# Kernel tuning notes

Hardware: AMD Instinct MI355X
Metric: run time of the kernel (lower is better)

The kernel has to match this reference:

```python
import jax, jax.numpy as jnp
import numpy as np

SPATIAL_SHAPES = [(100, 100), (50, 50), (25, 25), (13, 13)]  # (h, w) per level
D_MODEL, N_HEADS, N_LEVELS, N_POINTS = 256, 8, 4, 4
B = 2
S = sum(h * w for h, w in SPATIAL_SHAPES)  # 13294
Q = S  # encoder self-attention: num_queries == sequence_length


def setup_inputs() -> dict:
    key = jax.random.key(0)
    ks = jax.random.split(key, 12)
    d = D_MODEL
    hlp = N_HEADS * N_LEVELS * N_POINTS
    scale = 0.02
    starts = np.cumsum([0] + [h * w for h, w in SPATIAL_SHAPES[:-1]])
    return {
        "hidden_states": jax.random.normal(ks[0], (B, Q, d), jnp.float32),
        "encoder_hidden_states": jax.random.normal(ks[1], (B, S, d), jnp.float32),
        "reference_points": jax.random.uniform(ks[2], (B, Q, N_LEVELS, 2), jnp.float32),
        "W_value": jax.random.normal(ks[3], (d, d), jnp.float32) * scale,
        "b_value": jnp.zeros((d,), jnp.float32),
        "W_off": jax.random.normal(ks[4], (d, hlp * 2), jnp.float32) * scale,
        "b_off": jax.random.normal(ks[5], (hlp * 2,), jnp.float32) * scale,
        "W_attn": jax.random.normal(ks[6], (d, hlp), jnp.float32) * scale,
        "b_attn": jnp.zeros((hlp,), jnp.float32),
        "W_out": jax.random.normal(ks[7], (d, d), jnp.float32) * scale,
        "b_out": jnp.zeros((d,), jnp.float32),
        "spatial_shapes": jnp.asarray(SPATIAL_SHAPES, jnp.int32),
        "level_start_index": jnp.asarray(starts, jnp.int32),
    }


def bilinear_sample(img, grid):
    # img: [N, C, h, w]; grid: [N, Q, P, 2] xy in [-1, 1]
    # F.grid_sample(mode='bilinear', padding_mode='zeros', align_corners=False)
    N, C, h, w = img.shape
    Qg, Pg = grid.shape[1], grid.shape[2]
    x = ((grid[..., 0] + 1.0) * w - 1.0) * 0.5
    y = ((grid[..., 1] + 1.0) * h - 1.0) * 0.5
    x0 = jnp.floor(x)
    y0 = jnp.floor(y)
    x1 = x0 + 1.0
    y1 = y0 + 1.0
    wx1 = x - x0
    wx0 = 1.0 - wx1
    wy1 = y - y0
    wy0 = 1.0 - wy1
    img_flat = img.reshape(N, C, h * w)

    def gather(xi, yi):
        valid = (xi >= 0) & (xi <= w - 1) & (yi >= 0) & (yi <= h - 1)
        xi_c = jnp.clip(xi, 0, w - 1).astype(jnp.int32)
        yi_c = jnp.clip(yi, 0, h - 1).astype(jnp.int32)
        idx = (yi_c * w + xi_c).reshape(N, 1, Qg * Pg)
        vals = jnp.take_along_axis(img_flat, idx, axis=2)  # [N, C, Q*P]
        return vals * valid.reshape(N, 1, Qg * Pg).astype(img.dtype)

    out = (
        gather(x0, y0) * (wx0 * wy0).reshape(N, 1, -1)
        + gather(x1, y0) * (wx1 * wy0).reshape(N, 1, -1)
        + gather(x0, y1) * (wx0 * wy1).reshape(N, 1, -1)
        + gather(x1, y1) * (wx1 * wy1).reshape(N, 1, -1)
    )
    return out.reshape(N, C, Qg, Pg)


def reference(hidden_states, encoder_hidden_states, reference_points,
              W_value, b_value, W_off, b_off, W_attn, b_attn, W_out, b_out,
              spatial_shapes, level_start_index):
    Bq, Qn, d = hidden_states.shape
    H, L, P = N_HEADS, N_LEVELS, N_POINTS
    Dh = d // H
    value = (encoder_hidden_states @ W_value + b_value).reshape(Bq, -1, H, Dh)
    off = (hidden_states @ W_off + b_off).reshape(Bq, Qn, H, L, P, 2)
    aw = (hidden_states @ W_attn + b_attn).reshape(Bq, Qn, H, L * P)
    aw = jax.nn.softmax(aw, axis=-1).reshape(Bq, Qn, H, L, P)
    # offset normalizer is (width, height) per level
    norm = jnp.stack([spatial_shapes[:, 1], spatial_shapes[:, 0]], -1).astype(off.dtype)
    loc = reference_points[:, :, None, :, None, :] + off / norm[None, None, None, :, None, :]
    grids = 2.0 * loc - 1.0  # [B, Q, H, L, P, 2]

    starts = np.cumsum([0] + [h * w for h, w in SPATIAL_SHAPES])
    sampled = []
    for lvl, (h, w) in enumerate(SPATIAL_SHAPES):
        v = value[:, starts[lvl]:starts[lvl + 1]]              # [B, h*w, H, Dh]
        v = v.transpose(0, 2, 3, 1).reshape(Bq * H, Dh, h, w)   # [B*H, Dh, h, w]
        g = grids[:, :, :, lvl].transpose(0, 2, 1, 3, 4).reshape(Bq * H, Qn, P, 2)
        sampled.append(bilinear_sample(v, g))                   # [B*H, Dh, Q, P]
    samp = jnp.stack(sampled, axis=-2).reshape(Bq * H, Dh, Qn, L * P)
    wts = aw.transpose(0, 2, 1, 3, 4).reshape(Bq * H, 1, Qn, L * P)
    out = (samp * wts).sum(-1)                                  # [B*H, Dh, Q]
    out = out.reshape(Bq, H * Dh, Qn).transpose(0, 2, 1)        # [B, Q, d]
    out = out @ W_out + b_out
    return out, aw
```

## Files before the change

kernel.cpp:

```cpp
#include <hip/hip_runtime.h>
#include <hip/hip_bf16.h>
#include <math.h>

#define BQn 2
#define QN 13294
#define SN 13294
#define NH 8
#define DH 32
#define DM 256

typedef __attribute__((ext_vector_type(8))) short short8;
typedef __attribute__((ext_vector_type(4))) float f32x4;

__device__ __forceinline__ unsigned short f2bf(float x) {
    union { float f; unsigned int u; } c; c.f = x;
    unsigned int r = c.u + 0x7fff + ((c.u >> 16) & 1);
    return (unsigned short)(r >> 16);
}
__device__ __forceinline__ float asf(unsigned int u) {
    union { unsigned int i; float f; } c; c.i = u; return c.f;
}

__global__ __launch_bounds__(256) void conv_weights(
    const float* __restrict__ Wv, const float* __restrict__ Woff,
    const float* __restrict__ Wa, const float* __restrict__ Wout,
    unsigned short* __restrict__ WvT, unsigned short* __restrict__ WoffT,
    unsigned short* __restrict__ WaT, unsigned short* __restrict__ WoutT)
{
    const int t = blockIdx.x * 256 + threadIdx.x;
    if (t < 65536) {
        const int n = t & 255, k = t >> 8;
        WvT[(size_t)n * 256 + k] = f2bf(Wv[(size_t)k * 256 + n]);
    } else if (t < 131072) {
        const int i = t - 65536, n = i & 255, k = i >> 8;
        WoffT[(size_t)n * 256 + k] = f2bf(Woff[(size_t)k * 256 + n]);
    } else if (t < 163840) {
        const int i = t - 131072, n = i & 127, k = i >> 7;
        WaT[(size_t)n * 256 + k] = f2bf(Wa[(size_t)k * 128 + n]);
    } else if (t < 229376) {
        const int i = t - 163840, n = i & 255, k = i >> 8;
        WoutT[(size_t)n * 256 + k] = f2bf(Wout[(size_t)k * 256 + n]);
    }
}

template<int N, int MODE, bool AF32>
__global__ __launch_bounds__(256) void gemm_mfma(
    const void* __restrict__ Av,
    const unsigned short* __restrict__ WT,
    const float* __restrict__ bias0,
    const float* __restrict__ bias1,
    void* __restrict__ Cv, int M)
{
    __shared__ unsigned short As[128][72];
    __shared__ unsigned short Bs[64][72];
    const int tid  = threadIdx.x;
    const int lane = tid & 63, wid = tid >> 6;
    const int wr = wid >> 1, wc = wid & 1;
    const int r0 = blockIdx.y * 128, n0 = blockIdx.x * 64;

    f32x4 acc[4][2] = {};

    for (int k0 = 0; k0 < 256; k0 += 64) {
        #pragma unroll
        for (int i = 0; i < 4; ++i) {
            const int idx = i * 256 + tid;
            const int row = idx >> 3, ch = (idx & 7) << 3;
            int grow = r0 + row; if (grow >= M) grow = M - 1;
            if (AF32) {
                const float* Af = (const float*)Av;
                const float4 v0 = *(const float4*)(Af + (size_t)grow * 256 + k0 + ch);
                const float4 v1 = *(const float4*)(Af + (size_t)grow * 256 + k0 + ch + 4);
                union { __hip_bfloat162 b[4]; uint4 u; } pk;
                pk.b[0] = __float22bfloat162_rn(make_float2(v0.x, v0.y));
                pk.b[1] = __float22bfloat162_rn(make_float2(v0.z, v0.w));
                pk.b[2] = __float22bfloat162_rn(make_float2(v1.x, v1.y));
                pk.b[3] = __float22bfloat162_rn(make_float2(v1.z, v1.w));
                *(uint4*)&As[row][ch] = pk.u;
            } else {
                const unsigned short* Ab = (const unsigned short*)Av;
                *(uint4*)&As[row][ch] =
                    *(const uint4*)(Ab + (size_t)grow * 256 + k0 + ch);
            }
        }
        #pragma unroll
        for (int i = 0; i < 2; ++i) {
            const int idx = i * 256 + tid;
            const int row = idx >> 3, ch = (idx & 7) << 3;
            *(uint4*)&Bs[row][ch] =
                *(const uint4*)(WT + (size_t)(n0 + row) * 256 + k0 + ch);
        }
        __syncthreads();
        #pragma unroll
        for (int kk = 0; kk < 2; ++kk) {
            const int kb = kk * 32 + (lane >> 4) * 8;
            short8 bfr[2];
            #pragma unroll
            for (int n = 0; n < 2; ++n)
                bfr[n] = *(const short8*)&Bs[wc * 32 + n * 16 + (lane & 15)][kb];
            #pragma unroll
            for (int m = 0; m < 4; ++m) {
                const short8 afr =
                    *(const short8*)&As[wr * 64 + m * 16 + (lane & 15)][kb];
                #pragma unroll
                for (int n = 0; n < 2; ++n)
                    acc[m][n] = __builtin_amdgcn_mfma_f32_16x16x32_bf16(
                        afr, bfr[n], acc[m][n], 0, 0, 0);
            }
        }
        __syncthreads();
    }

    #pragma unroll
    for (int m = 0; m < 4; ++m)
        #pragma unroll
        for (int n = 0; n < 2; ++n) {
            const int col = n0 + wc * 32 + n * 16 + (lane & 15);
            const float bsv = (col < 256) ? bias0[col] : bias1[col - 256];
            #pragma unroll
            for (int j = 0; j < 4; ++j) {
                const int row = r0 + wr * 64 + m * 16 + (lane >> 4) * 4 + j;
                if (row >= M) continue;
                const float v = acc[m][n][j] + bsv;
                if (MODE == 0) {
                    ((float*)Cv)[(size_t)row * N + col] = v;
                } else {
                    const int b = (row >= SN), s = row - b * SN;
                    const int h = col >> 5, dh = col & 31;
                    ((unsigned short*)Cv)
                        [(((size_t)b * NH + h) * SN + s) * DH + dh] = f2bf(v);
                }
            }
        }
}

__global__ __launch_bounds__(256) void ms_sample(
    const unsigned short* __restrict__ value,
    const float* __restrict__ offaw,
    const float* __restrict__ refp,
    unsigned short* __restrict__ outh,
    float* __restrict__ awout)
{
    const int h  = blockIdx.x & 7;
    const int qc = blockIdx.x >> 3;
    const int lc = threadIdx.x & 7;
    const int bq = qc * 32 + (threadIdx.x >> 3);
    if (bq >= BQn * QN) return;
    const int b  = (bq >= QN);
    const int gbase = threadIdx.x & 56;

    const float* rowp = offaw + (size_t)bq * 384;

    const float2 lw2 = *(const float2*)(rowp + 256 + h * 16 + lc * 2);
    float m = fmaxf(lw2.x, lw2.y);
    #pragma unroll
    for (int d = 1; d < 8; d <<= 1) m = fmaxf(m, __shfl_xor(m, d, 8));
    float e0 = __expf(lw2.x - m), e1 = __expf(lw2.y - m);
    float s = e0 + e1;
    #pragma unroll
    for (int d = 1; d < 8; d <<= 1) s += __shfl_xor(s, d, 8);
    const float inv = 1.f / s;
    e0 *= inv; e1 *= inv;
    *(float2*)(awout + (size_t)bq * 128 + h * 16 + lc * 2) = make_float2(e0, e1);

    const float4 o4 = *(const float4*)(rowp + h * 32 + lc * 4);
    const int lvl = lc >> 1;
    const float2 rp = *(const float2*)(refp + (size_t)bq * 8 + lvl * 2);
    const float rw = (lvl == 0) ? 0.01f : (lvl == 1) ? 0.02f
                   : (lvl == 2) ? 0.04f : (1.0f / 13.0f);
    const float lx0 = fmaf(o4.x, rw, rp.x), ly0 = fmaf(o4.y, rw, rp.y);
    const float lx1 = fmaf(o4.z, rw, rp.x), ly1 = fmaf(o4.w, rw, rp.y);

    float ax = 0.f, ay = 0.f, az = 0.f, aw_ = 0.f;
    const unsigned short* vplane =
        value + (((size_t)b * NH + h) * SN) * DH + lc * 4;

    #pragma unroll
    for (int p = 0; p < 16; ++p) {
        constexpr int LW[4]  = {100, 50, 25, 13};
        constexpr int LST[4] = {0, 10000, 12500, 13125};
        const int l  = p >> 2;
        const int w  = LW[l];
        const int st = LST[l];
        const int src = gbase + (p >> 1);
        const float lx = __shfl((p & 1) ? lx1 : lx0, src, 64);
        const float ly = __shfl((p & 1) ? ly1 : ly0, src, 64);
        const float wt = __shfl((p & 1) ? e1  : e0,  src, 64);

        const float x = fmaf(lx, (float)w, -0.5f);
        const float y = fmaf(ly, (float)w, -0.5f);
        const float x0f = floorf(x), y0f = floorf(y);
        const int x0 = (int)x0f, y0 = (int)y0f;
        const float wx1 = x - x0f, wx0 = 1.f - wx1;
        const float wy1 = y - y0f, wy0 = 1.f - wy1;

        #pragma unroll
        for (int c = 0; c < 4; ++c) {
            const int xi = x0 + (c & 1);
            const int yi = y0 + (c >> 1);
            const float cw = ((c & 1) ? wx1 : wx0) * ((c >> 1) ? wy1 : wy0);
            const bool valid = ((unsigned)xi < (unsigned)w) &
                               ((unsigned)yi < (unsigned)w);
            const float wgt = valid ? cw * wt : 0.f;
            const int xc = min(max(xi, 0), w - 1);
            const int yc = min(max(yi, 0), w - 1);
            const uint2 v =
                *(const uint2*)(vplane + (size_t)(st + yc * w + xc) * DH);
            ax  = fmaf(wgt, asf(v.x << 16),          ax);
            ay  = fmaf(wgt, asf(v.x & 0xffff0000u),  ay);
            az  = fmaf(wgt, asf(v.y << 16),          az);
            aw_ = fmaf(wgt, asf(v.y & 0xffff0000u),  aw_);
        }
    }

    ushort4 o;
    o.x = f2bf(ax); o.y = f2bf(ay); o.z = f2bf(az); o.w = f2bf(aw_);
    *(ushort4*)(outh + (size_t)bq * 256 + h * 32 + lc * 4) = o;
}

extern "C" void kernel_launch(void* const* d_in, const int* in_sizes, int n_in,
                              void* d_out, int out_size, void* d_ws, size_t ws_size,
                              hipStream_t stream) {
    const float* hs   = (const float*)d_in[0];
    const float* enc  = (const float*)d_in[1];
    const float* refp = (const float*)d_in[2];
    const float* Wv   = (const float*)d_in[3];
    const float* bv   = (const float*)d_in[4];
    const float* Woff = (const float*)d_in[5];
    const float* boff = (const float*)d_in[6];
    const float* Wa   = (const float*)d_in[7];
    const float* ba   = (const float*)d_in[8];
    const float* Wout = (const float*)d_in[9];
    const float* bout = (const float*)d_in[10];

    float* out    = (float*)d_out;
    float* aw_out = out + (size_t)BQn * QN * 256;

    const size_t MQ = (size_t)BQn * QN;
    unsigned short* valueb = (unsigned short*)d_ws;
    float* offaw = (float*)(valueb + MQ * 256);
    unsigned short* outh  = (unsigned short*)(offaw + MQ * 384);
    unsigned short* WvT   = outh + MQ * 256;
    unsigned short* WcatT = WvT + 256 * 256;
    unsigned short* WoutT = WcatT + 384 * 256;

    const int M = (int)MQ;
    const dim3 blk(256);

    conv_weights<<<896, blk, 0, stream>>>(Wv, Woff, Wa, Wout,
                                          WvT, WcatT, WcatT + 65536, WoutT);

    const int my = (M + 127) / 128;
    gemm_mfma<256, 1, true ><<<dim3(4, my), blk, 0, stream>>>(
        enc, WvT, bv, bv, valueb, M);
    gemm_mfma<384, 0, true ><<<dim3(6, my), blk, 0, stream>>>(
        hs, WcatT, boff, ba, offaw, M);

    const int qchunks = (M + 31) / 32;
    ms_sample<<<8 * qchunks, blk, 0, stream>>>(valueb, offaw, refp,
                                               outh, aw_out);

    gemm_mfma<256, 0, false><<<dim3(4, my), blk, 0, stream>>>(
        outh, WoutT, bout, bout, out, M);
}
```

Measured before the change: 142.8 us.

## Widen GEMM N-tile to 128 and give each sampler thread 8 channels

The GEMM tile grows from 128x64 to 128x128, so each block reads the fp32 A rows (with their bf16 conversion) half as many times, at the cost of more accumulator registers and fewer blocks. The sampling kernel now maps 4 threads per query-head instead of 8, with each thread loading 16-byte chunks covering 8 channels and handling one level's softmax and offsets. This halves the sampler's thread count, widens its gathers and needs fewer shuffles, but each thread now carries more registers and latency.

New measurement: 445.1 us. +211.7%, slower.

```diff
diff --git a/kernel.cpp b/kernel.cpp
--- a/kernel.cpp
+++ b/kernel.cpp
@@ -52,13 +52,13 @@
     void* __restrict__ Cv, int M)
 {
     __shared__ unsigned short As[128][72];
-    __shared__ unsigned short Bs[64][72];
+    __shared__ unsigned short Bs[128][72];
     const int tid  = threadIdx.x;
     const int lane = tid & 63, wid = tid >> 6;
     const int wr = wid >> 1, wc = wid & 1;
-    const int r0 = blockIdx.y * 128, n0 = blockIdx.x * 64;
-
-    f32x4 acc[4][2] = {};
+    const int r0 = blockIdx.y * 128, n0 = blockIdx.x * 128;
+
+    f32x4 acc[4][4] = {};
 
     for (int k0 = 0; k0 < 256; k0 += 64) {
         #pragma unroll
@@ -83,7 +83,7 @@
             }
         }
         #pragma unroll
-        for (int i = 0; i < 2; ++i) {
+        for (int i = 0; i < 4; ++i) {
             const int idx = i * 256 + tid;
             const int row = idx >> 3, ch = (idx & 7) << 3;
             *(uint4*)&Bs[row][ch] =
@@ -93,16 +93,16 @@
         #pragma unroll
         for (int kk = 0; kk < 2; ++kk) {
             const int kb = kk * 32 + (lane >> 4) * 8;
-            short8 bfr[2];
+            short8 bfr[4];
             #pragma unroll
-            for (int n = 0; n < 2; ++n)
-                bfr[n] = *(const short8*)&Bs[wc * 32 + n * 16 + (lane & 15)][kb];
+            for (int n = 0; n < 4; ++n)
+                bfr[n] = *(const short8*)&Bs[wc * 64 + n * 16 + (lane & 15)][kb];
             #pragma unroll
             for (int m = 0; m < 4; ++m) {
                 const short8 afr =
                     *(const short8*)&As[wr * 64 + m * 16 + (lane & 15)][kb];
                 #pragma unroll
-                for (int n = 0; n < 2; ++n)
+                for (int n = 0; n < 4; ++n)
                     acc[m][n] = __builtin_amdgcn_mfma_f32_16x16x32_bf16(
                         afr, bfr[n], acc[m][n], 0, 0, 0);
             }
@@ -113,8 +113,8 @@
     #pragma unroll
     for (int m = 0; m < 4; ++m)
         #pragma unroll
-        for (int n = 0; n < 2; ++n) {
-            const int col = n0 + wc * 32 + n * 16 + (lane & 15);
+        for (int n = 0; n < 4; ++n) {
+            const int col = n0 + wc * 64 + n * 16 + (lane & 15);
             const float bsv = (col < 256) ? bias0[col] : bias1[col - 256];
             #pragma unroll
             for (int j = 0; j < 4; ++j) {
@@ -142,37 +142,42 @@
 {
     const int h  = blockIdx.x & 7;
     const int qc = blockIdx.x >> 3;
-    const int lc = threadIdx.x & 7;
-    const int bq = qc * 32 + (threadIdx.x >> 3);
+    const int lc = threadIdx.x & 3;
+    const int bq = qc * 64 + (threadIdx.x >> 2);
     if (bq >= BQn * QN) return;
     const int b  = (bq >= QN);
-    const int gbase = threadIdx.x & 56;
+    const int gbase = threadIdx.x & 60;
 
     const float* rowp = offaw + (size_t)bq * 384;
 
-    const float2 lw2 = *(const float2*)(rowp + 256 + h * 16 + lc * 2);
-    float m = fmaxf(lw2.x, lw2.y);
-    #pragma unroll
-    for (int d = 1; d < 8; d <<= 1) m = fmaxf(m, __shfl_xor(m, d, 8));
-    float e0 = __expf(lw2.x - m), e1 = __expf(lw2.y - m);
-    float s = e0 + e1;
-    #pragma unroll
-    for (int d = 1; d < 8; d <<= 1) s += __shfl_xor(s, d, 8);
+    const float4 lg = *(const float4*)(rowp + 256 + h * 16 + lc * 4);
+    float m = fmaxf(fmaxf(lg.x, lg.y), fmaxf(lg.z, lg.w));
+    m = fmaxf(m, __shfl_xor(m, 1, 4));
+    m = fmaxf(m, __shfl_xor(m, 2, 4));
+    float e0 = __expf(lg.x - m), e1 = __expf(lg.y - m),
+          e2 = __expf(lg.z - m), e3 = __expf(lg.w - m);
+    float s = (e0 + e1) + (e2 + e3);
+    s += __shfl_xor(s, 1, 4);
+    s += __shfl_xor(s, 2, 4);
     const float inv = 1.f / s;
-    e0 *= inv; e1 *= inv;
-    *(float2*)(awout + (size_t)bq * 128 + h * 16 + lc * 2) = make_float2(e0, e1);
-
-    const float4 o4 = *(const float4*)(rowp + h * 32 + lc * 4);
-    const int lvl = lc >> 1;
-    const float2 rp = *(const float2*)(refp + (size_t)bq * 8 + lvl * 2);
-    const float rw = (lvl == 0) ? 0.01f : (lvl == 1) ? 0.02f
-                   : (lvl == 2) ? 0.04f : (1.0f / 13.0f);
-    const float lx0 = fmaf(o4.x, rw, rp.x), ly0 = fmaf(o4.y, rw, rp.y);
-    const float lx1 = fmaf(o4.z, rw, rp.x), ly1 = fmaf(o4.w, rw, rp.y);
-
-    float ax = 0.f, ay = 0.f, az = 0.f, aw_ = 0.f;
+    e0 *= inv; e1 *= inv; e2 *= inv; e3 *= inv;
+    *(float4*)(awout + (size_t)bq * 128 + h * 16 + lc * 4) =
+        make_float4(e0, e1, e2, e3);
+
+    const float4 oa = *(const float4*)(rowp + h * 32 + lc * 8);
+    const float4 ob = *(const float4*)(rowp + h * 32 + lc * 8 + 4);
+    const float2 rp = *(const float2*)(refp + (size_t)bq * 8 + lc * 2);
+    const float rw = (lc == 0) ? 0.01f : (lc == 1) ? 0.02f
+                   : (lc == 2) ? 0.04f : (1.0f / 13.0f);
+    const float lx0 = fmaf(oa.x, rw, rp.x), ly0 = fmaf(oa.y, rw, rp.y);
+    const float lx1 = fmaf(oa.z, rw, rp.x), ly1 = fmaf(oa.w, rw, rp.y);
+    const float lx2 = fmaf(ob.x, rw, rp.x), ly2 = fmaf(ob.y, rw, rp.y);
+    const float lx3 = fmaf(ob.z, rw, rp.x), ly3 = fmaf(ob.w, rw, rp.y);
+
+    float a0 = 0.f, a1 = 0.f, a2 = 0.f, a3 = 0.f,
+          a4 = 0.f, a5 = 0.f, a6 = 0.f, a7 = 0.f;
     const unsigned short* vplane =
-        value + (((size_t)b * NH + h) * SN) * DH + lc * 4;
+        value + (((size_t)b * NH + h) * SN) * DH + lc * 8;
 
     #pragma unroll
     for (int p = 0; p < 16; ++p) {
@@ -181,10 +186,11 @@
         const int l  = p >> 2;
         const int w  = LW[l];
         const int st = LST[l];
-        const int src = gbase + (p >> 1);
-        const float lx = __shfl((p & 1) ? lx1 : lx0, src, 64);
-        const float ly = __shfl((p & 1) ? ly1 : ly0, src, 64);
-        const float wt = __shfl((p & 1) ? e1  : e0,  src, 64);
+        const int src = gbase + l;
+        const int pi = p & 3;
+        const float lx = __shfl(pi == 0 ? lx0 : pi == 1 ? lx1 : pi == 2 ? lx2 : lx3, src, 64);
+        const float ly = __shfl(pi == 0 ? ly0 : pi == 1 ? ly1 : pi == 2 ? ly2 : ly3, src, 64);
+        const float wt = __shfl(pi == 0 ? e0  : pi == 1 ? e1  : pi == 2 ? e2  : e3,  src, 64);
 
         const float x = fmaf(lx, (float)w, -0.5f);
         const float y = fmaf(ly, (float)w, -0.5f);
@@ -203,18 +209,23 @@
             const float wgt = valid ? cw * wt : 0.f;
             const int xc = min(max(xi, 0), w - 1);
             const int yc = min(max(yi, 0), w - 1);
-            const uint2 v =
-                *(const uint2*)(vplane + (size_t)(st + yc * w + xc) * DH);
-            ax  = fmaf(wgt, asf(v.x << 16),          ax);
-            ay  = fmaf(wgt, asf(v.x & 0xffff0000u),  ay);
-            az  = fmaf(wgt, asf(v.y << 16),          az);
-            aw_ = fmaf(wgt, asf(v.y & 0xffff0000u),  aw_);
+            const uint4 v =
+                *(const uint4*)(vplane + (size_t)(st + yc * w + xc) * DH);
+            a0 = fmaf(wgt, asf(v.x << 16),         a0);
+            a1 = fmaf(wgt, asf(v.x & 0xffff0000u), a1);
+            a2 = fmaf(wgt, asf(v.y << 16),         a2);
+            a3 = fmaf(wgt, asf(v.y & 0xffff0000u), a3);
+            a4 = fmaf(wgt, asf(v.z << 16),         a4);
+            a5 = fmaf(wgt, asf(v.z & 0xffff0000u), a5);
+            a6 = fmaf(wgt, asf(v.w << 16),         a6);
+            a7 = fmaf(wgt, asf(v.w & 0xffff0000u), a7);
         }
     }
 
-    ushort4 o;
-    o.x = f2bf(ax); o.y = f2bf(ay); o.z = f2bf(az); o.w = f2bf(aw_);
-    *(ushort4*)(outh + (size_t)bq * 256 + h * 32 + lc * 4) = o;
+    union { unsigned short us[8]; uint4 u; } o;
+    o.us[0] = f2bf(a0); o.us[1] = f2bf(a1); o.us[2] = f2bf(a2); o.us[3] = f2bf(a3);
+    o.us[4] = f2bf(a4); o.us[5] = f2bf(a5); o.us[6] = f2bf(a6); o.us[7] = f2bf(a7);
+    *(uint4*)(outh + (size_t)bq * 256 + h * 32 + lc * 8) = o.u;
 }
 
 extern "C" void kernel_launch(void* const* d_in, const int* in_sizes, int n_in,
@@ -250,15 +261,15 @@
                                           WvT, WcatT, WcatT + 65536, WoutT);
 
     const int my = (M + 127) / 128;
-    gemm_mfma<256, 1, true ><<<dim3(4, my), blk, 0, stream>>>(
+    gemm_mfma<256, 1, true ><<<dim3(2, my), blk, 0, stream>>>(
         enc, WvT, bv, bv, valueb, M);
-    gemm_mfma<384, 0, true ><<<dim3(6, my), blk, 0, stream>>>(
+    gemm_mfma<384, 0, true ><<<dim3(3, my), blk, 0, stream>>>(
         hs, WcatT, boff, ba, offaw, M);
 
-    const int qchunks = (M + 31) / 32;
+    const int qchunks = (M + 63) / 64;
     ms_sample<<<8 * qchunks, blk, 0, stream>>>(valueb, offaw, refp,
                                                outh, aw_out);
 
-    gemm_mfma<256, 0, false><<<dim3(4, my), blk, 0, stream>>>(
+    gemm_mfma<256, 0, false><<<dim3(2, my), blk, 0, stream>>>(
         outh, WoutT, bout, bout, out, M);
 }
```
